# Performance work log

Hardware: AMD Instinct MI355X
Metric: run time of the kernel (lower is better)

## Reference

```python
import jax, jax.numpy as jnp
import numpy as np

N, E, IN, H, G = 20000, 640000, 64, 128, 64
EPS = 1e-5


def _ln(x, g, b):
    m = x.mean(-1, keepdims=True)
    v = ((x - m) ** 2).mean(-1, keepdims=True)
    return (x - m) / jnp.sqrt(v + EPS) * g + b


def _edge_softmax(a, dst):
    # softmax over incoming edges of each destination node, per channel
    m = jax.lax.stop_gradient(jax.ops.segment_max(a, dst, num_segments=N))
    m = jnp.where(jnp.isfinite(m), m, 0.0)
    e = jnp.exp(a - m[dst])
    s = jax.ops.segment_sum(e, dst, num_segments=N)
    return e / s[dst]


def setup_inputs():
    key = jax.random.key(0)
    ks = jax.random.split(key, 32)
    nrm = lambda k, sh, s=1.0: jax.random.normal(k, sh, jnp.float32) * s
    w = 0.05  # weight init scale
    inp = {
        'kind': nrm(ks[0], (N, IN)),
        'ntype': nrm(ks[1], (N, IN)),
        'eh': nrm(ks[2], (E, IN)),
        'Qw': nrm(ks[3], (2 * IN, H), w), 'Qb': jnp.zeros((H,), jnp.float32),
        'Kw': nrm(ks[4], (3 * IN, H), w), 'Kb': jnp.zeros((H,), jnp.float32),
        'Vw': nrm(ks[5], (3 * IN, H), w), 'Vb': jnp.zeros((H,), jnp.float32),
        'Ww': nrm(ks[6], (H + 2 * IN, H), w), 'Wb': jnp.zeros((H,), jnp.float32),
        'Q2w': nrm(ks[7], (2 * IN + H, H), w), 'Q2b': jnp.zeros((H,), jnp.float32),
        'K2w': nrm(ks[8], (3 * IN + H, H), w), 'K2b': jnp.zeros((H,), jnp.float32),
        'V2w': nrm(ks[9], (3 * IN + H, H), w), 'V2b': jnp.zeros((H,), jnp.float32),
        'W2w': nrm(ks[10], (2 * H + 2 * IN, H), w), 'W2b': jnp.zeros((H,), jnp.float32),
        'ln_g': jnp.ones((H,), jnp.float32), 'ln_b': jnp.zeros((H,), jnp.float32),
        'gate_w': nrm(ks[11], (H, 1), w), 'gate_b': jnp.zeros((1,), jnp.float32),
        'src': jax.random.randint(ks[12], (E,), 0, N, jnp.int32),
        'dst': jax.random.randint(ks[13], (E,), 0, N, jnp.int32),
        'gid': jnp.sort(jax.random.randint(ks[14], (N,), 0, G, jnp.int32)),
    }
    return inp


def reference(kind, ntype, eh, Qw, Qb, Kw, Kb, Vw, Vb, Ww, Wb, Q2w, Q2b,
              K2w, K2b, V2w, V2b, W2w, W2b, ln_g, ln_b, gate_w, gate_b,
              src, dst, gid):
    # ---- layer 1 ----
    q = jnp.concatenate([kind, ntype], 1) @ Qw + Qb                 # [N,H]
    ek = jnp.concatenate([kind[src], ntype[src], eh], 1)            # [E,3IN]
    k = ek @ Kw + Kb                                                # [E,H]
    v = ek @ Vw + Vb                                                # [E,H]
    alpha = _edge_softmax(q[dst] * k, dst)                          # v_mul_e + edge_softmax
    h_n = jax.ops.segment_sum(alpha * v, dst, num_segments=N)      # scatter-sum
    h = _ln(jnp.concatenate([h_n, kind, ntype], 1) @ Ww + Wb, ln_g, ln_b)
    # ---- layer 2 ----
    q2 = jnp.concatenate([kind, ntype, h], 1) @ Q2w + Q2b
    ek2 = jnp.concatenate([kind[src], ntype[src], eh, h[src]], 1)
    k2 = ek2 @ K2w + K2b
    v2 = ek2 @ V2w + V2b
    alpha2 = _edge_softmax(q2[dst] * k2, dst)
    h_n1 = jax.ops.segment_sum(alpha2 * v2, dst, num_segments=N)
    h1 = _ln(jnp.concatenate([h_n1, h, kind, ntype], 1) @ W2w + W2b, ln_g, ln_b)
    # ---- global attention pooling readout ----
    logit = h1 @ gate_w + gate_b                                    # [N,1]
    gm = jax.lax.stop_gradient(jax.ops.segment_max(logit, gid, num_segments=G))
    ge = jnp.exp(logit - gm[gid])
    gs = jax.ops.segment_sum(ge, gid, num_segments=G)
    gate = ge / gs[gid]
    return jax.ops.segment_sum(gate * h1, gid, num_segments=G)     # [G,H]
```

## Files before the change

### kernel.cpp

```cpp
#include <hip/hip_runtime.h>
#include <math.h>

#define NN   20000
#define NE   640000
#define NPADN 20480
#define HH   128
#define GG   64
#define INF_ 1e30f
#define FB2  4096

typedef unsigned short u16;
typedef short bf16x8 __attribute__((ext_vector_type(8)));
typedef float f32x4 __attribute__((ext_vector_type(4)));

struct KMap { int colb[12]; };

__device__ __forceinline__ u16 f2bf(float x) {
  union { float f; unsigned u; } c; c.f = x;
  unsigned r = c.u + 0x7FFFu + ((c.u >> 16) & 1u);
  return (u16)(r >> 16);
}
__device__ __forceinline__ float bflo(unsigned w) {
  union { unsigned u; float f; } c; c.u = w << 16; return c.f;
}
__device__ __forceinline__ float bfhi(unsigned w) {
  union { unsigned u; float f; } c; c.u = w & 0xFFFF0000u; return c.f;
}

__device__ __forceinline__ float blk_sum(float v, float* red) {
#pragma unroll
  for (int off = 32; off >= 1; off >>= 1) v += __shfl_xor(v, off);
  if ((threadIdx.x & 63) == 0) red[threadIdx.x >> 6] = v;
  __syncthreads();
  float r = red[0] + red[1];
  __syncthreads();
  return r;
}
__device__ __forceinline__ float blk_max(float v, float* red) {
#pragma unroll
  for (int off = 32; off >= 1; off >>= 1) v = fmaxf(v, __shfl_xor(v, off));
  if ((threadIdx.x & 63) == 0) red[threadIdx.x >> 6] = v;
  __syncthreads();
  float r = fmaxf(red[0], red[1]);
  __syncthreads();
  return r;
}

__global__ void zero_ints(int* p, int n) {
  int i = blockIdx.x * 256 + threadIdx.x;
  if (i < n) p[i] = 0;
}

__global__ void hist_kernel(const int* __restrict__ dst, int* __restrict__ deg) {
  int e = blockIdx.x * 256 + threadIdx.x;
  if (e < NE) atomicAdd(&deg[dst[e]], 1);
}

__global__ void scan_kernel(const int* __restrict__ deg, int* __restrict__ row_start,
                            int* __restrict__ cursor) {
  __shared__ int buf[256];
  __shared__ int carry_s;
  int t = threadIdx.x;
  if (t == 0) carry_s = 0;
  __syncthreads();
  for (int base = 0; base < NPADN; base += 4096) {
    int idx0 = base + t * 16;
    int4 a = *(const int4*)&deg[idx0];
    int4 b = *(const int4*)&deg[idx0 + 4];
    int4 c = *(const int4*)&deg[idx0 + 8];
    int4 d = *(const int4*)&deg[idx0 + 12];
    int x[16] = {a.x,a.y,a.z,a.w, b.x,b.y,b.z,b.w, c.x,c.y,c.z,c.w, d.x,d.y,d.z,d.w};
    int pre[16];
    int run = 0;
#pragma unroll
    for (int j = 0; j < 16; j++) { pre[j] = run; run += x[j]; }
    buf[t] = run;
    __syncthreads();
    int sum = run;
#pragma unroll
    for (int off = 1; off < 256; off <<= 1) {
      int addv = (t >= off) ? buf[t - off] : 0;
      __syncthreads();
      sum += addv;
      buf[t] = sum;
      __syncthreads();
    }
    int excl = sum - run;
    int carry = carry_s;
    int basev = carry + excl;
#pragma unroll
    for (int j = 0; j < 16; j++) {
      int i = idx0 + j;
      if (i < NN) { row_start[i] = basev + pre[j]; cursor[i] = basev + pre[j]; }
    }
    __syncthreads();
    if (t == 255) carry_s = carry + sum;
    __syncthreads();
  }
  if (t == 0) row_start[NN] = carry_s;
}

__global__ void scatter_kernel(const int* __restrict__ dst, const int* __restrict__ src,
                               int* __restrict__ cursor, int2* __restrict__ se) {
  int e = blockIdx.x * 256 + threadIdx.x;
  if (e < NE) {
    int d = dst[e];
    int p = atomicAdd(&cursor[d], 1);
    int2 v; v.x = src[e]; v.y = e;
    se[p] = v;
  }
}

__global__ __launch_bounds__(256) void ehb_pack(const float* __restrict__ eh,
                                                u16* __restrict__ ehb) {
  int t = blockIdx.x * 256 + threadIdx.x;
  int p = t >> 3, l = t & 7;
  if (p < NE) {
    const float* r = eh + (size_t)p * 64 + l * 8;
    float4 a = *(const float4*)r;
    float4 b = *(const float4*)(r + 4);
    union { u16 u[8]; uint4 v; } pk;
    pk.u[0] = f2bf(a.x); pk.u[1] = f2bf(a.y); pk.u[2] = f2bf(a.z); pk.u[3] = f2bf(a.w);
    pk.u[4] = f2bf(b.x); pk.u[5] = f2bf(b.y); pk.u[6] = f2bf(b.z); pk.u[7] = f2bf(b.w);
    *(uint4*)&ehb[(size_t)p * 64 + l * 8] = pk.v;
  }
}

__global__ void pack_x(const float* __restrict__ kind, const float* __restrict__ ntype,
                       u16* __restrict__ XM) {
  int i = blockIdx.x * 256 + threadIdx.x;
  if (i < NN * 128) {
    int n = i >> 7, c = i & 127;
    float v = (c < 64) ? kind[n * 64 + c] : ntype[n * 64 + (c - 64)];
    XM[(size_t)n * 512 + c] = f2bf(v);
  }
}

__global__ void pack_wt(const float* __restrict__ W, u16* __restrict__ dst, int K,
                        int skip_at, int skip_amt) {
  int i = blockIdx.x * 256 + threadIdx.x;
  if (i < 128 * K) {
    int c = i / K, k = i - c * K;
    int row = (k < skip_at) ? k : k + skip_amt;
    dst[i] = f2bf(W[row * 128 + c]);
  }
}

__global__ void wtrans(const float* __restrict__ W, u16* __restrict__ Wt) {
  int i = blockIdx.x * 256 + threadIdx.x;
  if (i < 128 * 64) {
    int c = i >> 6, k = i & 63;
    Wt[i] = f2bf(W[k * 128 + c]);
  }
}

template <int KSTEPS, bool DO_LN, bool DO_LOGIT>
__global__ __launch_bounds__(256) void mfma_gemm(
    const u16* __restrict__ XM, const u16* __restrict__ Wt, KMap kmap,
    const float* __restrict__ b0, const float* __restrict__ b1, const float* __restrict__ b2,
    float* __restrict__ o0, u16* __restrict__ kvB, u16* __restrict__ outbf,
    const float* __restrict__ ln_g, const float* __restrict__ ln_b,
    const float* __restrict__ gate_w, const float* __restrict__ gate_b,
    float* __restrict__ logit) {
  const int lane = threadIdx.x & 63;
  const int wv = threadIdx.x >> 6;
  const int er = lane & 15, kg = lane >> 4;
  const int row0 = (blockIdx.x * 4 + wv) * 16;
  if (row0 >= NN) return;
  const int chunk = blockIdx.y;
  const int arow = (row0 + er < NN) ? row0 + er : NN - 1;
  constexpr int K = KSTEPS * 32;
  const u16* aptr = XM + (size_t)arow * 512 + kg * 8;
  const u16* wptr = Wt + (size_t)chunk * 128 * K + (size_t)er * K + kg * 8;

  f32x4 acc[8];
#pragma unroll
  for (int i = 0; i < 8; i++) acc[i] = (f32x4){0.f, 0.f, 0.f, 0.f};

#pragma unroll
  for (int ks = 0; ks < KSTEPS; ks++) {
    bf16x8 a = *(const bf16x8*)&aptr[kmap.colb[ks]];
#pragma unroll
    for (int nt = 0; nt < 8; nt++) {
      bf16x8 b = *(const bf16x8*)&wptr[(size_t)nt * 16 * K + ks * 32];
      acc[nt] = __builtin_amdgcn_mfma_f32_16x16x32_bf16(a, b, acc[nt], 0, 0, 0);
    }
  }

  if (!DO_LN) {
    const float* bp = (chunk == 0) ? b0 : (chunk == 1) ? b1 : b2;
#pragma unroll
    for (int t = 0; t < 8; t++) {
      int col = er + 16 * t;
      float bv = bp[col];
#pragma unroll
      for (int r = 0; r < 4; r++) {
        int m = row0 + kg * 4 + r;
        if (m < NN) {
          float val = acc[t][r] + bv;
          if (chunk == 0) o0[(size_t)m * 128 + col] = val;
          else            kvB[(size_t)m * 256 + 2 * col + (chunk - 1)] = f2bf(val);
        }
      }
    }
  } else {
    float g[8], bb[8], gw[8];
#pragma unroll
    for (int t = 0; t < 8; t++) {
      int col = er + 16 * t;
      float bv = b0[col];
#pragma unroll
      for (int r = 0; r < 4; r++) acc[t][r] += bv;
      g[t] = ln_g[col]; bb[t] = ln_b[col];
      if (DO_LOGIT) gw[t] = gate_w[col];
    }
    float gb0 = DO_LOGIT ? gate_b[0] : 0.f;
#pragma unroll
    for (int r = 0; r < 4; r++) {
      float s = 0.f;
#pragma unroll
      for (int t = 0; t < 8; t++) s += acc[t][r];
#pragma unroll
      for (int off = 1; off <= 8; off <<= 1) s += __shfl_xor(s, off);
      float mean = s * (1.0f / 128.0f);
      float v = 0.f;
#pragma unroll
      for (int t = 0; t < 8; t++) { float d = acc[t][r] - mean; v = fmaf(d, d, v); }
#pragma unroll
      for (int off = 1; off <= 8; off <<= 1) v += __shfl_xor(v, off);
      float rstd = 1.0f / sqrtf(v * (1.0f / 128.0f) + 1e-5f);
      int m = row0 + kg * 4 + r;
      float lg = 0.f;
      float hv[8];
#pragma unroll
      for (int t = 0; t < 8; t++) {
        hv[t] = (acc[t][r] - mean) * rstd * g[t] + bb[t];
        if (DO_LOGIT) lg = fmaf(hv[t], gw[t], lg);
      }
      if (m < NN) {
        if (outbf) {
#pragma unroll
          for (int t = 0; t < 8; t++) outbf[(size_t)m * 512 + er + 16 * t] = f2bf(hv[t]);
        } else {
#pragma unroll
          for (int t = 0; t < 8; t++) o0[(size_t)m * 128 + er + 16 * t] = hv[t];
        }
      }
      if (DO_LOGIT) {
#pragma unroll
        for (int off = 1; off <= 8; off <<= 1) lg += __shfl_xor(lg, off);
        if (er == 0 && m < NN) logit[m] = lg + gb0;
      }
    }
  }
}

#define PIDX(S, t_) { \
    int pp = rs + (t_) * 16 + er; \
    int lv = (pp < re) ? 1 : 0; \
    int pq = lv ? pp : re - 1; \
    pcv##S = pq < 0 ? 0 : pq; \
    pmN##S = lv ? 1.f : 0.f; \
    int2 sev = se[pcv##S]; \
    srcv##S = sev.x; eidx##S = sev.y; }

#define PEHB(S) { \
    const u16* ep_ = ehb + (size_t)eidx##S * 64 + kg * 8; \
    bE0##S = *(const bf16x8*)&ep_[0]; \
    bE1##S = *(const bf16x8*)&ep_[32]; }

#define PGKV(S) { \
    const u16* kp_ = kvb + (size_t)srcv##S * 256 + 2 * cbase; \
    kv0##S = *(const uint4*)&kp_[0]; \
    kv1##S = *(const uint4*)&kp_[32]; }

#define PCOMP(S) { \
    f32x4 cK0 = {0.f,0.f,0.f,0.f}, cK1 = {0.f,0.f,0.f,0.f}; \
    f32x4 cV0 = {0.f,0.f,0.f,0.f}, cV1 = {0.f,0.f,0.f,0.f}; \
    cK0 = __builtin_amdgcn_mfma_f32_16x16x32_bf16(aK00, bE0##S, cK0, 0, 0, 0); \
    cK0 = __builtin_amdgcn_mfma_f32_16x16x32_bf16(aK01, bE1##S, cK0, 0, 0, 0); \
    cK1 = __builtin_amdgcn_mfma_f32_16x16x32_bf16(aK10, bE0##S, cK1, 0, 0, 0); \
    cK1 = __builtin_amdgcn_mfma_f32_16x16x32_bf16(aK11, bE1##S, cK1, 0, 0, 0); \
    cV0 = __builtin_amdgcn_mfma_f32_16x16x32_bf16(aV00, bE0##S, cV0, 0, 0, 0); \
    cV0 = __builtin_amdgcn_mfma_f32_16x16x32_bf16(aV01, bE1##S, cV0, 0, 0, 0); \
    cV1 = __builtin_amdgcn_mfma_f32_16x16x32_bf16(aV10, bE0##S, cV1, 0, 0, 0); \
    cV1 = __builtin_amdgcn_mfma_f32_16x16x32_bf16(aV11, bE1##S, cV1, 0, 0, 0); \
    float pm = pmC##S; \
    float kk, vv, pe; \
    kk = bflo(kv0##S.x) + cK0[0]; vv = bfhi(kv0##S.x) + cV0[0]; \
    pe = __expf(q0v.x * kk) * pm; S0[0] += pe; H0[0] = fmaf(pe, vv, H0[0]); \
    kk = bflo(kv0##S.y) + cK0[1]; vv = bfhi(kv0##S.y) + cV0[1]; \
    pe = __expf(q0v.y * kk) * pm; S0[1] += pe; H0[1] = fmaf(pe, vv, H0[1]); \
    kk = bflo(kv0##S.z) + cK0[2]; vv = bfhi(kv0##S.z) + cV0[2]; \
    pe = __expf(q0v.z * kk) * pm; S0[2] += pe; H0[2] = fmaf(pe, vv, H0[2]); \
    kk = bflo(kv0##S.w) + cK0[3]; vv = bfhi(kv0##S.w) + cV0[3]; \
    pe = __expf(q0v.w * kk) * pm; S0[3] += pe; H0[3] = fmaf(pe, vv, H0[3]); \
    kk = bflo(kv1##S.x) + cK1[0]; vv = bfhi(kv1##S.x) + cV1[0]; \
    pe = __expf(q1v.x * kk) * pm; S1[0] += pe; H1[0] = fmaf(pe, vv, H1[0]); \
    kk = bflo(kv1##S.y) + cK1[1]; vv = bfhi(kv1##S.y) + cV1[1]; \
    pe = __expf(q1v.y * kk) * pm; S1[1] += pe; H1[1] = fmaf(pe, vv, H1[1]); \
    kk = bflo(kv1##S.z) + cK1[2]; vv = bfhi(kv1##S.z) + cV1[2]; \
    pe = __expf(q1v.z * kk) * pm; S1[2] += pe; H1[2] = fmaf(pe, vv, H1[2]); \
    kk = bflo(kv1##S.w) + cK1[3]; vv = bfhi(kv1##S.w) + cV1[3]; \
    pe = __expf(q1v.w * kk) * pm; S1[3] += pe; H1[3] = fmaf(pe, vv, H1[3]); }

__global__ __launch_bounds__(256, 3) void edge_fused(
    const u16* __restrict__ ehb, const int2* __restrict__ se,
    const int* __restrict__ row_start,
    const u16* __restrict__ WtK, const u16* __restrict__ WtV,
    const float* __restrict__ qn, const u16* __restrict__ kvb,
    u16* __restrict__ xmh) {
  const int lane = threadIdx.x & 63;
  const int qw = threadIdx.x >> 6;
  const int er = lane & 15, kg = lane >> 4;
  const int cbase = qw * 32 + kg * 4;

  bf16x8 aK00, aK01, aK10, aK11, aV00, aV01, aV10, aV11;
  {
    int r0 = (qw * 2 + 0) * 16 + er;
    int r1 = (qw * 2 + 1) * 16 + er;
    aK00 = *(const bf16x8*)&WtK[r0 * 64 + kg * 8];
    aK01 = *(const bf16x8*)&WtK[r0 * 64 + 32 + kg * 8];
    aK10 = *(const bf16x8*)&WtK[r1 * 64 + kg * 8];
    aK11 = *(const bf16x8*)&WtK[r1 * 64 + 32 + kg * 8];
    aV00 = *(const bf16x8*)&WtV[r0 * 64 + kg * 8];
    aV01 = *(const bf16x8*)&WtV[r0 * 64 + 32 + kg * 8];
    aV10 = *(const bf16x8*)&WtV[r1 * 64 + kg * 8];
    aV11 = *(const bf16x8*)&WtV[r1 * 64 + 32 + kg * 8];
  }

  for (int n = blockIdx.x; n < NN; n += FB2) {
    const int rs = row_start[n], re = row_start[n + 1];
    const int T2 = (re - rs + 15) >> 4;
    float4 q0v = *(const float4*)&qn[(size_t)n * 128 + cbase];
    float4 q1v = *(const float4*)&qn[(size_t)n * 128 + cbase + 16];
    f32x4 S0 = {0.f,0.f,0.f,0.f}, S1 = {0.f,0.f,0.f,0.f};
    f32x4 H0 = {0.f,0.f,0.f,0.f}, H1 = {0.f,0.f,0.f,0.f};

    int pcvA, srcvA, eidxA, pcvB, srcvB, eidxB, pcvC, srcvC, eidxC;
    float pmNA, pmCA, pmNB, pmCB, pmNC, pmCC;
    bf16x8 bE0A, bE1A, bE0B, bE1B, bE0C, bE1C;
    uint4 kv0A, kv1A, kv0B, kv1B, kv0C, kv1C;

    PIDX(A, 0); pmCA = pmNA; PEHB(A); PGKV(A);
    PIDX(B, 1); pmCB = pmNB; PEHB(B); PGKV(B);
    PIDX(C, 2); pmCC = pmNC; PEHB(C); PGKV(C);

    for (int t = 0; t < T2; t += 3) {
      PIDX(A, t + 3); PCOMP(A); pmCA = pmNA; PEHB(A); PGKV(A);
      PIDX(B, t + 4); PCOMP(B); pmCB = pmNB; PEHB(B); PGKV(B);
      PIDX(C, t + 5); PCOMP(C); pmCC = pmNC; PEHB(C); PGKV(C);
    }

#pragma unroll
    for (int off = 1; off <= 8; off <<= 1) {
#pragma unroll
      for (int j = 0; j < 4; j++) {
        S0[j] += __shfl_xor(S0[j], off);
        H0[j] += __shfl_xor(H0[j], off);
        S1[j] += __shfl_xor(S1[j], off);
        H1[j] += __shfl_xor(H1[j], off);
      }
    }
    if (er == 0) {
      uint2 p0, p1;
      if (re > rs) {
        p0.x = (unsigned)f2bf(H0[0]/S0[0]) | ((unsigned)f2bf(H0[1]/S0[1]) << 16);
        p0.y = (unsigned)f2bf(H0[2]/S0[2]) | ((unsigned)f2bf(H0[3]/S0[3]) << 16);
        p1.x = (unsigned)f2bf(H1[0]/S1[0]) | ((unsigned)f2bf(H1[1]/S1[1]) << 16);
        p1.y = (unsigned)f2bf(H1[2]/S1[2]) | ((unsigned)f2bf(H1[3]/S1[3]) << 16);
      } else { p0.x = p0.y = p1.x = p1.y = 0u; }
      *(uint2*)&xmh[(size_t)n * 512 + cbase] = p0;
      *(uint2*)&xmh[(size_t)n * 512 + cbase + 16] = p1;
    }
  }
}

__global__ void gstart_kernel(const int* __restrict__ gid, int* __restrict__ gstart) {
  int g = threadIdx.x;
  if (g <= GG) {
    int lo = 0, hi = NN;
    while (lo < hi) {
      int mid = (lo + hi) >> 1;
      if (gid[mid] < g) lo = mid + 1; else hi = mid;
    }
    gstart[g] = lo;
  }
}

__global__ __launch_bounds__(128) void readout_kernel(
    const float* __restrict__ h1, const float* __restrict__ logit,
    const int* __restrict__ gstart, float* __restrict__ out) {
  __shared__ float red[2];
  int g = blockIdx.x, tid = threadIdx.x;
  int s0 = gstart[g], s1 = gstart[g + 1];

  float mx = -INF_;
  for (int i = s0 + tid; i < s1; i += 128) mx = fmaxf(mx, logit[i]);
  mx = blk_max(mx, red);

  float sum = 0.0f;
  for (int i = s0 + tid; i < s1; i += 128) sum += __expf(logit[i] - mx);
  sum = blk_sum(sum, red);

  float acc = 0.0f;
  for (int i = s0; i < s1; i++) {
    float w = __expf(logit[i] - mx);
    acc = fmaf(w, h1[i * 128 + tid], acc);
  }
  out[g * 128 + tid] = (s1 > s0) ? (acc / sum) : 0.0f;
}

extern "C" void kernel_launch(void* const* d_in, const int* in_sizes, int n_in,
                              void* d_out, int out_size, void* d_ws, size_t ws_size,
                              hipStream_t stream) {
  const float* kind  = (const float*)d_in[0];
  const float* ntype = (const float*)d_in[1];
  const float* eh    = (const float*)d_in[2];
  const float* Qw = (const float*)d_in[3];  const float* Qb = (const float*)d_in[4];
  const float* Kw = (const float*)d_in[5];  const float* Kb = (const float*)d_in[6];
  const float* Vw = (const float*)d_in[7];  const float* Vb = (const float*)d_in[8];
  const float* Ww = (const float*)d_in[9];  const float* Wb = (const float*)d_in[10];
  const float* Q2w = (const float*)d_in[11]; const float* Q2b = (const float*)d_in[12];
  const float* K2w = (const float*)d_in[13]; const float* K2b = (const float*)d_in[14];
  const float* V2w = (const float*)d_in[15]; const float* V2b = (const float*)d_in[16];
  const float* W2w = (const float*)d_in[17]; const float* W2b = (const float*)d_in[18];
  const float* ln_g = (const float*)d_in[19]; const float* ln_b = (const float*)d_in[20];
  const float* gate_w = (const float*)d_in[21]; const float* gate_b = (const float*)d_in[22];
  const int* src = (const int*)d_in[23];
  const int* dst = (const int*)d_in[24];
  const int* gid = (const int*)d_in[25];
  float* out = (float*)d_out;

  char* wp = (char*)d_ws;
  auto alloc = [&](size_t bytes) {
    void* p = (void*)wp;
    wp += (bytes + 255) & ~(size_t)255;
    return p;
  };
  u16* XM  = (u16*)alloc((size_t)NN * 512 * 2);
  u16* ehb = (u16*)alloc((size_t)NE * 64 * 2);
  float* qA = (float*)alloc((size_t)NN * HH * 4);
  u16* kvB = (u16*)alloc((size_t)NN * 256 * 2);
  float* h1 = (float*)alloc((size_t)NN * HH * 4);
  float* logit = (float*)alloc((size_t)NN * 4);
  u16* Wt1 = (u16*)alloc((size_t)384 * 128 * 2);
  u16* Wt2 = (u16*)alloc((size_t)128 * 256 * 2);
  u16* Wt3 = (u16*)alloc((size_t)384 * 256 * 2);
  u16* Wt4 = (u16*)alloc((size_t)128 * 384 * 2);
  u16* WtK1 = (u16*)alloc((size_t)128 * 64 * 2);
  u16* WtV1 = (u16*)alloc((size_t)128 * 64 * 2);
  u16* WtK2 = (u16*)alloc((size_t)128 * 64 * 2);
  u16* WtV2 = (u16*)alloc((size_t)128 * 64 * 2);
  int* deg       = (int*)alloc((size_t)NPADN * 4);
  int* row_start = (int*)alloc((size_t)(NN + 1) * 4);
  int* cursor    = (int*)alloc((size_t)NN * 4);
  int2* se       = (int2*)alloc((size_t)NE * 8);
  int* gstart    = (int*)alloc((size_t)(GG + 1) * 4);

  const int NB = 1 << 30;

  zero_ints<<<(NPADN + 255) / 256, 256, 0, stream>>>(deg, NPADN);
  hist_kernel<<<(NE + 255) / 256, 256, 0, stream>>>(dst, deg);
  scan_kernel<<<1, 256, 0, stream>>>(deg, row_start, cursor);
  scatter_kernel<<<(NE + 255) / 256, 256, 0, stream>>>(dst, src, cursor, se);
  ehb_pack<<<(NE * 8 + 255) / 256, 256, 0, stream>>>(eh, ehb);

  pack_x<<<(NN * 128 + 255) / 256, 256, 0, stream>>>(kind, ntype, XM);
  pack_wt<<<(128 * 128 + 255) / 256, 256, 0, stream>>>(Qw, Wt1, 128, NB, 0);
  pack_wt<<<(128 * 128 + 255) / 256, 256, 0, stream>>>(Kw, Wt1 + 128 * 128, 128, NB, 0);
  pack_wt<<<(128 * 128 + 255) / 256, 256, 0, stream>>>(Vw, Wt1 + 2 * 128 * 128, 128, NB, 0);
  pack_wt<<<(128 * 256 + 255) / 256, 256, 0, stream>>>(Ww, Wt2, 256, NB, 0);
  pack_wt<<<(128 * 256 + 255) / 256, 256, 0, stream>>>(Q2w, Wt3, 256, NB, 0);
  pack_wt<<<(128 * 256 + 255) / 256, 256, 0, stream>>>(K2w, Wt3 + 128 * 256, 256, 128, 64);
  pack_wt<<<(128 * 256 + 255) / 256, 256, 0, stream>>>(V2w, Wt3 + 2 * 128 * 256, 256, 128, 64);
  pack_wt<<<(128 * 384 + 255) / 256, 256, 0, stream>>>(W2w, Wt4, 384, NB, 0);
  wtrans<<<32, 256, 0, stream>>>(Kw + 128 * 128, WtK1);
  wtrans<<<32, 256, 0, stream>>>(Vw + 128 * 128, WtV1);
  wtrans<<<32, 256, 0, stream>>>(K2w + 128 * 128, WtK2);
  wtrans<<<32, 256, 0, stream>>>(V2w + 128 * 128, WtV2);

  KMap km1{}, km2{}, km3{}, km4{};
  for (int b = 0; b < 4; b++)  km1.colb[b] = 32 * b;
  for (int b = 0; b < 8; b++)  km2.colb[b] = (b < 4) ? 128 + 32 * b : 32 * (b - 4);
  for (int b = 0; b < 8; b++)  km3.colb[b] = (b < 4) ? 32 * b : 256 + 32 * (b - 4);
  for (int b = 0; b < 12; b++) km4.colb[b] = (b < 4) ? 384 + 32 * b
                                       : (b < 8) ? 256 + 32 * (b - 4) : 32 * (b - 8);

  const int GB = (NN + 63) / 64;

  mfma_gemm<4, false, false><<<dim3(GB, 3), 256, 0, stream>>>(
      XM, Wt1, km1, Qb, Kb, Vb, qA, kvB, nullptr,
      nullptr, nullptr, nullptr, nullptr, nullptr);

  edge_fused<<<FB2, 256, 0, stream>>>(ehb, se, row_start, WtK1, WtV1,
                                      qA, kvB, XM + 128);

  mfma_gemm<8, true, false><<<dim3(GB, 1), 256, 0, stream>>>(
      XM, Wt2, km2, Wb, nullptr, nullptr, nullptr, nullptr, XM + 256,
      ln_g, ln_b, nullptr, nullptr, nullptr);

  mfma_gemm<8, false, false><<<dim3(GB, 3), 256, 0, stream>>>(
      XM, Wt3, km3, Q2b, K2b, V2b, qA, kvB, nullptr,
      nullptr, nullptr, nullptr, nullptr, nullptr);

  edge_fused<<<FB2, 256, 0, stream>>>(ehb, se, row_start, WtK2, WtV2,
                                      qA, kvB, XM + 384);

  mfma_gemm<12, true, true><<<dim3(GB, 1), 256, 0, stream>>>(
      XM, Wt4, km4, W2b, nullptr, nullptr, h1, nullptr, nullptr,
      ln_g, ln_b, gate_w, gate_b, logit);

  gstart_kernel<<<1, 128, 0, stream>>>(gid, gstart);
  readout_kernel<<<GG, 128, 0, stream>>>(h1, logit, gstart, out);
}
```

Measured before the change: 664.1 us.

## Process two destination nodes per block in edge kernel with interleaved tiles

The fused edge kernel now handles a pair of destination nodes (n and n+10000) per block iteration. It interleaves their 16-edge tiles through the same three-stage prefetch pipeline, keeping separate softmax accumulators per node and selecting q per tile. Launch bounds rise to four blocks per SM and the grid shrinks to 2500. The aim is to amortise per-node prologue and pipeline fill and to keep more loads in flight, at the cost of more registers, doubled accumulation FMAs per element, and padding to the longer of the two rows. The readout loop is also unrolled by four with independent accumulators to expose ILP.

```diff
diff --git a/kernel.cpp b/kernel.cpp
--- a/kernel.cpp
+++ b/kernel.cpp
@@ -2,12 +2,13 @@
 #include <math.h>
 
 #define NN   20000
+#define NN2  10000
 #define NE   640000
 #define NPADN 20480
 #define HH   128
 #define GG   64
 #define INF_ 1e30f
-#define FB2  4096
+#define FBP  2500
 
 typedef unsigned short u16;
 typedef short bf16x8 __attribute__((ext_vector_type(8)));
@@ -255,12 +256,17 @@
   }
 }
 
-#define PIDX(S, t_) { \
-    int pp = rs + (t_) * 16 + er; \
-    int lv = (pp < re) ? 1 : 0; \
-    int pq = lv ? pp : re - 1; \
-    pcv##S = pq < 0 ? 0 : pq; \
-    pmN##S = lv ? 1.f : 0.f; \
+#define PIDX(S, p_) { \
+    int isA_ = (((p_) & 1) == 0); \
+    int tile_ = (p_) >> 1; \
+    int rs_ = isA_ ? rsA : rsB; \
+    int re_ = isA_ ? reA : reB; \
+    int pp = rs_ + tile_ * 16 + er; \
+    float pm_ = (pp < re_) ? 1.f : 0.f; \
+    pcv##S = pp < NE - 1 ? pp : NE - 1; \
+    mAN##S = isA_ ? pm_ : 0.f; \
+    mBN##S = isA_ ? 0.f : pm_; \
+    selN##S = isA_; \
     int2 sev = se[pcv##S]; \
     srcv##S = sev.x; eidx##S = sev.y; }
 
@@ -273,6 +279,17 @@
     const u16* kp_ = kvb + (size_t)srcv##S * 256 + 2 * cbase; \
     kv0##S = *(const uint4*)&kp_[0]; \
     kv1##S = *(const uint4*)&kp_[32]; }
+
+#define PROLL(S) { mAC##S = mAN##S; mBC##S = mBN##S; selC##S = selN##S; }
+
+#define PCH(S, KV, CK, CV, QA, QB, SA, HA, SB, HB, comp) { \
+    float kk = bflo(KV.comp) + CK; \
+    float vv = bfhi(KV.comp) + CV; \
+    float q_ = selC##S ? QA : QB; \
+    float pe = __expf(q_ * kk); \
+    float peA = pe * mAC##S, peB = pe * mBC##S; \
+    SA += peA; HA = fmaf(peA, vv, HA); \
+    SB += peB; HB = fmaf(peB, vv, HB); }
 
 #define PCOMP(S) { \
     f32x4 cK0 = {0.f,0.f,0.f,0.f}, cK1 = {0.f,0.f,0.f,0.f}; \
@@ -285,26 +302,16 @@
     cV0 = __builtin_amdgcn_mfma_f32_16x16x32_bf16(aV01, bE1##S, cV0, 0, 0, 0); \
     cV1 = __builtin_amdgcn_mfma_f32_16x16x32_bf16(aV10, bE0##S, cV1, 0, 0, 0); \
     cV1 = __builtin_amdgcn_mfma_f32_16x16x32_bf16(aV11, bE1##S, cV1, 0, 0, 0); \
-    float pm = pmC##S; \
-    float kk, vv, pe; \
-    kk = bflo(kv0##S.x) + cK0[0]; vv = bfhi(kv0##S.x) + cV0[0]; \
-    pe = __expf(q0v.x * kk) * pm; S0[0] += pe; H0[0] = fmaf(pe, vv, H0[0]); \
-    kk = bflo(kv0##S.y) + cK0[1]; vv = bfhi(kv0##S.y) + cV0[1]; \
-    pe = __expf(q0v.y * kk) * pm; S0[1] += pe; H0[1] = fmaf(pe, vv, H0[1]); \
-    kk = bflo(kv0##S.z) + cK0[2]; vv = bfhi(kv0##S.z) + cV0[2]; \
-    pe = __expf(q0v.z * kk) * pm; S0[2] += pe; H0[2] = fmaf(pe, vv, H0[2]); \
-    kk = bflo(kv0##S.w) + cK0[3]; vv = bfhi(kv0##S.w) + cV0[3]; \
-    pe = __expf(q0v.w * kk) * pm; S0[3] += pe; H0[3] = fmaf(pe, vv, H0[3]); \
-    kk = bflo(kv1##S.x) + cK1[0]; vv = bfhi(kv1##S.x) + cV1[0]; \
-    pe = __expf(q1v.x * kk) * pm; S1[0] += pe; H1[0] = fmaf(pe, vv, H1[0]); \
-    kk = bflo(kv1##S.y) + cK1[1]; vv = bfhi(kv1##S.y) + cV1[1]; \
-    pe = __expf(q1v.y * kk) * pm; S1[1] += pe; H1[1] = fmaf(pe, vv, H1[1]); \
-    kk = bflo(kv1##S.z) + cK1[2]; vv = bfhi(kv1##S.z) + cV1[2]; \
-    pe = __expf(q1v.z * kk) * pm; S1[2] += pe; H1[2] = fmaf(pe, vv, H1[2]); \
-    kk = bflo(kv1##S.w) + cK1[3]; vv = bfhi(kv1##S.w) + cV1[3]; \
-    pe = __expf(q1v.w * kk) * pm; S1[3] += pe; H1[3] = fmaf(pe, vv, H1[3]); }
-
-__global__ __launch_bounds__(256, 3) void edge_fused(
+    PCH(S, kv0##S, cK0[0], cV0[0], qA0.x, qB0.x, SA0[0], HA0[0], SB0[0], HB0[0], x); \
+    PCH(S, kv0##S, cK0[1], cV0[1], qA0.y, qB0.y, SA0[1], HA0[1], SB0[1], HB0[1], y); \
+    PCH(S, kv0##S, cK0[2], cV0[2], qA0.z, qB0.z, SA0[2], HA0[2], SB0[2], HB0[2], z); \
+    PCH(S, kv0##S, cK0[3], cV0[3], qA0.w, qB0.w, SA0[3], HA0[3], SB0[3], HB0[3], w); \
+    PCH(S, kv1##S, cK1[0], cV1[0], qA1.x, qB1.x, SA1[0], HA1[0], SB1[0], HB1[0], x); \
+    PCH(S, kv1##S, cK1[1], cV1[1], qA1.y, qB1.y, SA1[1], HA1[1], SB1[1], HB1[1], y); \
+    PCH(S, kv1##S, cK1[2], cV1[2], qA1.z, qB1.z, SA1[2], HA1[2], SB1[2], HB1[2], z); \
+    PCH(S, kv1##S, cK1[3], cV1[3], qA1.w, qB1.w, SA1[3], HA1[3], SB1[3], HB1[3], w); }
+
+__global__ __launch_bounds__(256, 4) void edge_fused(
     const u16* __restrict__ ehb, const int2* __restrict__ se,
     const int* __restrict__ row_start,
     const u16* __restrict__ WtK, const u16* __restrict__ WtV,
@@ -329,49 +336,70 @@
     aV11 = *(const bf16x8*)&WtV[r1 * 64 + 32 + kg * 8];
   }
 
-  for (int n = blockIdx.x; n < NN; n += FB2) {
-    const int rs = row_start[n], re = row_start[n + 1];
-    const int T2 = (re - rs + 15) >> 4;
-    float4 q0v = *(const float4*)&qn[(size_t)n * 128 + cbase];
-    float4 q1v = *(const float4*)&qn[(size_t)n * 128 + cbase + 16];
-    f32x4 S0 = {0.f,0.f,0.f,0.f}, S1 = {0.f,0.f,0.f,0.f};
-    f32x4 H0 = {0.f,0.f,0.f,0.f}, H1 = {0.f,0.f,0.f,0.f};
-
-    int pcvA, srcvA, eidxA, pcvB, srcvB, eidxB, pcvC, srcvC, eidxC;
-    float pmNA, pmCA, pmNB, pmCB, pmNC, pmCC;
-    bf16x8 bE0A, bE1A, bE0B, bE1B, bE0C, bE1C;
-    uint4 kv0A, kv1A, kv0B, kv1B, kv0C, kv1C;
-
-    PIDX(A, 0); pmCA = pmNA; PEHB(A); PGKV(A);
-    PIDX(B, 1); pmCB = pmNB; PEHB(B); PGKV(B);
-    PIDX(C, 2); pmCC = pmNC; PEHB(C); PGKV(C);
-
-    for (int t = 0; t < T2; t += 3) {
-      PIDX(A, t + 3); PCOMP(A); pmCA = pmNA; PEHB(A); PGKV(A);
-      PIDX(B, t + 4); PCOMP(B); pmCB = pmNB; PEHB(B); PGKV(B);
-      PIDX(C, t + 5); PCOMP(C); pmCC = pmNC; PEHB(C); PGKV(C);
+  for (int m = blockIdx.x; m < NN2; m += FBP) {
+    const int nA = m, nB = m + NN2;
+    const int rsA = row_start[nA], reA = row_start[nA + 1];
+    const int rsB = row_start[nB], reB = row_start[nB + 1];
+    const int TA = (reA - rsA + 15) >> 4, TB = (reB - rsB + 15) >> 4;
+    const int T = TA > TB ? TA : TB;
+    float4 qA0 = *(const float4*)&qn[(size_t)nA * 128 + cbase];
+    float4 qA1 = *(const float4*)&qn[(size_t)nA * 128 + cbase + 16];
+    float4 qB0 = *(const float4*)&qn[(size_t)nB * 128 + cbase];
+    float4 qB1 = *(const float4*)&qn[(size_t)nB * 128 + cbase + 16];
+    f32x4 SA0 = {0.f,0.f,0.f,0.f}, SA1 = {0.f,0.f,0.f,0.f};
+    f32x4 HA0 = {0.f,0.f,0.f,0.f}, HA1 = {0.f,0.f,0.f,0.f};
+    f32x4 SB0 = {0.f,0.f,0.f,0.f}, SB1 = {0.f,0.f,0.f,0.f};
+    f32x4 HB0 = {0.f,0.f,0.f,0.f}, HB1 = {0.f,0.f,0.f,0.f};
+
+    int pcvX, srcvX, eidxX, pcvY, srcvY, eidxY, pcvZ, srcvZ, eidxZ;
+    int selNX, selCX, selNY, selCY, selNZ, selCZ;
+    float mANX, mACX, mBNX, mBCX, mANY, mACY, mBNY, mBCY, mANZ, mACZ, mBNZ, mBCZ;
+    bf16x8 bE0X, bE1X, bE0Y, bE1Y, bE0Z, bE1Z;
+    uint4 kv0X, kv1X, kv0Y, kv1Y, kv0Z, kv1Z;
+
+    PIDX(X, 0); PROLL(X); PEHB(X); PGKV(X);
+    PIDX(Y, 1); PROLL(Y); PEHB(Y); PGKV(Y);
+    PIDX(Z, 2); PROLL(Z); PEHB(Z); PGKV(Z);
+
+    const int PEND = 2 * T;
+    for (int p = 0; p < PEND; p += 3) {
+      PIDX(X, p + 3); PCOMP(X); PROLL(X); PEHB(X); PGKV(X);
+      PIDX(Y, p + 4); PCOMP(Y); PROLL(Y); PEHB(Y); PGKV(Y);
+      PIDX(Z, p + 5); PCOMP(Z); PROLL(Z); PEHB(Z); PGKV(Z);
     }
 
 #pragma unroll
     for (int off = 1; off <= 8; off <<= 1) {
 #pragma unroll
       for (int j = 0; j < 4; j++) {
-        S0[j] += __shfl_xor(S0[j], off);
-        H0[j] += __shfl_xor(H0[j], off);
-        S1[j] += __shfl_xor(S1[j], off);
-        H1[j] += __shfl_xor(H1[j], off);
+        SA0[j] += __shfl_xor(SA0[j], off);
+        HA0[j] += __shfl_xor(HA0[j], off);
+        SA1[j] += __shfl_xor(SA1[j], off);
+        HA1[j] += __shfl_xor(HA1[j], off);
+        SB0[j] += __shfl_xor(SB0[j], off);
+        HB0[j] += __shfl_xor(HB0[j], off);
+        SB1[j] += __shfl_xor(SB1[j], off);
+        HB1[j] += __shfl_xor(HB1[j], off);
       }
     }
     if (er == 0) {
       uint2 p0, p1;
-      if (re > rs) {
-        p0.x = (unsigned)f2bf(H0[0]/S0[0]) | ((unsigned)f2bf(H0[1]/S0[1]) << 16);
-        p0.y = (unsigned)f2bf(H0[2]/S0[2]) | ((unsigned)f2bf(H0[3]/S0[3]) << 16);
-        p1.x = (unsigned)f2bf(H1[0]/S1[0]) | ((unsigned)f2bf(H1[1]/S1[1]) << 16);
-        p1.y = (unsigned)f2bf(H1[2]/S1[2]) | ((unsigned)f2bf(H1[3]/S1[3]) << 16);
+      if (reA > rsA) {
+        p0.x = (unsigned)f2bf(HA0[0]/SA0[0]) | ((unsigned)f2bf(HA0[1]/SA0[1]) << 16);
+        p0.y = (unsigned)f2bf(HA0[2]/SA0[2]) | ((unsigned)f2bf(HA0[3]/SA0[3]) << 16);
+        p1.x = (unsigned)f2bf(HA1[0]/SA1[0]) | ((unsigned)f2bf(HA1[1]/SA1[1]) << 16);
+        p1.y = (unsigned)f2bf(HA1[2]/SA1[2]) | ((unsigned)f2bf(HA1[3]/SA1[3]) << 16);
       } else { p0.x = p0.y = p1.x = p1.y = 0u; }
-      *(uint2*)&xmh[(size_t)n * 512 + cbase] = p0;
-      *(uint2*)&xmh[(size_t)n * 512 + cbase + 16] = p1;
+      *(uint2*)&xmh[(size_t)nA * 512 + cbase] = p0;
+      *(uint2*)&xmh[(size_t)nA * 512 + cbase + 16] = p1;
+      if (reB > rsB) {
+        p0.x = (unsigned)f2bf(HB0[0]/SB0[0]) | ((unsigned)f2bf(HB0[1]/SB0[1]) << 16);
+        p0.y = (unsigned)f2bf(HB0[2]/SB0[2]) | ((unsigned)f2bf(HB0[3]/SB0[3]) << 16);
+        p1.x = (unsigned)f2bf(HB1[0]/SB1[0]) | ((unsigned)f2bf(HB1[1]/SB1[1]) << 16);
+        p1.y = (unsigned)f2bf(HB1[2]/SB1[2]) | ((unsigned)f2bf(HB1[3]/SB1[3]) << 16);
+      } else { p0.x = p0.y = p1.x = p1.y = 0u; }
+      *(uint2*)&xmh[(size_t)nB * 512 + cbase] = p0;
+      *(uint2*)&xmh[(size_t)nB * 512 + cbase + 16] = p1;
     }
   }
 }
@@ -403,11 +431,23 @@
   for (int i = s0 + tid; i < s1; i += 128) sum += __expf(logit[i] - mx);
   sum = blk_sum(sum, red);
 
-  float acc = 0.0f;
-  for (int i = s0; i < s1; i++) {
+  float a0 = 0.f, a1 = 0.f, a2 = 0.f, a3 = 0.f;
+  int i = s0;
+  for (; i + 4 <= s1; i += 4) {
+    float w0 = __expf(logit[i + 0] - mx);
+    float w1 = __expf(logit[i + 1] - mx);
+    float w2 = __expf(logit[i + 2] - mx);
+    float w3 = __expf(logit[i + 3] - mx);
+    a0 = fmaf(w0, h1[(size_t)(i + 0) * 128 + tid], a0);
+    a1 = fmaf(w1, h1[(size_t)(i + 1) * 128 + tid], a1);
+    a2 = fmaf(w2, h1[(size_t)(i + 2) * 128 + tid], a2);
+    a3 = fmaf(w3, h1[(size_t)(i + 3) * 128 + tid], a3);
+  }
+  for (; i < s1; i++) {
     float w = __expf(logit[i] - mx);
-    acc = fmaf(w, h1[i * 128 + tid], acc);
-  }
+    a0 = fmaf(w, h1[(size_t)i * 128 + tid], a0);
+  }
+  float acc = (a0 + a1) + (a2 + a3);
   out[g * 128 + tid] = (s1 > s0) ? (acc / sum) : 0.0f;
 }
 
@@ -493,7 +533,7 @@
       XM, Wt1, km1, Qb, Kb, Vb, qA, kvB, nullptr,
       nullptr, nullptr, nullptr, nullptr, nullptr);
 
-  edge_fused<<<FB2, 256, 0, stream>>>(ehb, se, row_start, WtK1, WtV1,
+  edge_fused<<<FBP, 256, 0, stream>>>(ehb, se, row_start, WtK1, WtV1,
                                       qA, kvB, XM + 128);
 
   mfma_gemm<8, true, false><<<dim3(GB, 1), 256, 0, stream>>>(
@@ -504,7 +544,7 @@
       XM, Wt3, km3, Q2b, K2b, V2b, qA, kvB, nullptr,
       nullptr, nullptr, nullptr, nullptr, nullptr);
 
-  edge_fused<<<FB2, 256, 0, stream>>>(ehb, se, row_start, WtK2, WtV2,
+  edge_fused<<<FBP, 256, 0, stream>>>(ehb, se, row_start, WtK2, WtV2,
                                       qA, kvB, XM + 384);
 
   mfma_gemm<12, true, true><<<dim3(GB, 1), 256, 0, stream>>>(
```

Result: slower. 1.162 ms (+75.0%).
